# Kernel tuning notes

Hardware: AMD Instinct MI355X
Metric: run time of the kernel (lower is better)

Reference implementation:

```python
import jax, jax.numpy as jnp
import numpy as np

N_NODES = 100000
N_EDGES = 3200000
STATE_DIM = 128
HIDDEN = 256
ACTION_DIM = 64
BN_EPS = 1e-5


def setup_inputs() -> dict:
    key = jax.random.key(0)
    ks = jax.random.split(key, 12)
    feat = jax.random.normal(ks[0], (N_NODES, STATE_DIM), dtype=jnp.float32)
    src = jax.random.randint(ks[1], (N_EDGES,), 0, N_NODES, dtype=jnp.int64) if jax.config.jax_enable_x64 else jax.random.randint(ks[1], (N_EDGES,), 0, N_NODES).astype(jnp.int32)
    dst = jax.random.randint(ks[2], (N_EDGES,), 0, N_NODES).astype(src.dtype)
    def glorot(k, shape):
        lim = np.sqrt(6.0 / (shape[0] + shape[1]))
        return jax.random.uniform(k, shape, jnp.float32, -lim, lim)
    W1 = glorot(ks[3], (STATE_DIM, HIDDEN)); b1 = jnp.zeros((HIDDEN,), jnp.float32)
    W2 = glorot(ks[4], (HIDDEN, HIDDEN));   b2 = jnp.zeros((HIDDEN,), jnp.float32)
    g1 = jnp.ones((HIDDEN,), jnp.float32);  be1 = jnp.zeros((HIDDEN,), jnp.float32)
    g2 = jnp.ones((HIDDEN,), jnp.float32);  be2 = jnp.zeros((HIDDEN,), jnp.float32)
    Wa = glorot(ks[5], (HIDDEN, ACTION_DIM)); ba = jnp.zeros((ACTION_DIM,), jnp.float32)
    Wv = glorot(ks[6], (HIDDEN, 1));          bv = jnp.zeros((1,), jnp.float32)
    return {"feat": feat, "src": src, "dst": dst, "W1": W1, "b1": b1, "g1": g1, "be1": be1,
            "W2": W2, "b2": b2, "g2": g2, "be2": be2, "Wa": Wa, "ba": ba, "Wv": Wv, "bv": bv}


def _graph_conv(x, src, dst, dnorm_out, dnorm_in, W, b):
    # DGL GraphConv, norm='both': scale by out-deg^{-1/2} at src, sum-aggregate at dst,
    # scale by in-deg^{-1/2}, then linear.
    m = x * dnorm_out[:, None]                     # [N, F]
    agg = jax.ops.segment_sum(m[src], dst, num_segments=N_NODES)  # SpMM
    h = agg * dnorm_in[:, None]
    return h @ W + b


def _bn_relu(x, gamma, beta):
    mu = x.mean(axis=0)
    var = x.var(axis=0)  # biased, matches torch BN training normalization
    return jax.nn.relu((x - mu) * jax.lax.rsqrt(var + BN_EPS) * gamma + beta)


def reference(feat, src, dst, W1, b1, g1, be1, W2, b2, g2, be2, Wa, ba, Wv, bv):
    ones = jnp.ones((src.shape[0],), feat.dtype)
    deg_out = jax.ops.segment_sum(ones, src, num_segments=N_NODES)
    deg_in = jax.ops.segment_sum(ones, dst, num_segments=N_NODES)
    dnorm_out = jax.lax.rsqrt(jnp.clip(deg_out, 1.0))
    dnorm_in = jax.lax.rsqrt(jnp.clip(deg_in, 1.0))
    h = _bn_relu(_graph_conv(feat, src, dst, dnorm_out, dnorm_in, W1, b1), g1, be1)
    h = _bn_relu(_graph_conv(h, src, dst, dnorm_out, dnorm_in, W2, b2), g2, be2)
    adv = h @ Wa + ba                              # [N, A]
    val = h @ Wv + bv                              # [N, 1]
    Q = val + (adv - adv.mean(axis=1, keepdims=True))
    return Q
```

## Files before the change

### kernel.cpp

```cpp
#include <hip/hip_runtime.h>
#include <hip/hip_bf16.h>

#define NN 100000
#define NE 3200000
#define HID 256
#define SDIM 128
#define ADIM 64
#define BN_EPS 1e-5f

#define BSH 9
#define NB 196
#define EPB 8192
#define NAB 391

typedef __attribute__((ext_vector_type(8))) short short8;
typedef __attribute__((ext_vector_type(4))) float f32x4;

__device__ __forceinline__ void atomAdd(float* p, float v) { unsafeAtomicAdd(p, v); }
__device__ __forceinline__ float bf2f(ushort u) {
    union { unsigned i; float f; } c; c.i = ((unsigned)u) << 16; return c.f;
}
__device__ __forceinline__ ushort f2bf(float x) {
    __hip_bfloat16 h = __float2bfloat16(x);
    return *reinterpret_cast<ushort*>(&h);
}

__global__ __launch_bounds__(1024)
void k_hist(const int* __restrict__ src, const int* __restrict__ dst,
            unsigned* __restrict__ gh_d, unsigned* __restrict__ gh_s, int E) {
    __shared__ unsigned hd[NB], hs[NB];
    int tid = threadIdx.x;
    if (tid < NB) { hd[tid] = 0; hs[tid] = 0; }
    __syncthreads();
    int base = blockIdx.x * EPB;
    int cnt = min(EPB, E - base);
    for (int i = tid; i < cnt; i += 1024) {
        atomicAdd(&hd[dst[base + i] >> BSH], 1u);
        atomicAdd(&hs[src[base + i] >> BSH], 1u);
    }
    __syncthreads();
    if (tid < NB) {
        if (hd[tid]) atomicAdd(&gh_d[tid * 16], hd[tid]);
        if (hs[tid]) atomicAdd(&gh_s[tid * 16], hs[tid]);
    }
}

__global__ __launch_bounds__(256)
void k_scan_b(const unsigned* __restrict__ gh_d, const unsigned* __restrict__ gh_s,
              unsigned* __restrict__ gcur_d, unsigned* __restrict__ gcur_s,
              unsigned* __restrict__ bbase_d, unsigned* __restrict__ bbase_s,
              int* __restrict__ row_ptr) {
    __shared__ unsigned v[256];
    int t = threadIdx.x;
    unsigned x = (t < NB) ? gh_d[t * 16] : 0;
    v[t] = x; __syncthreads();
    for (int off = 1; off < 256; off <<= 1) {
        unsigned a = (t >= off) ? v[t - off] : 0;
        __syncthreads(); v[t] += a; __syncthreads();
    }
    if (t < NB) { bbase_d[t] = v[t] - x; gcur_d[t * 16] = v[t] - x; }
    if (t == 255) { bbase_d[NB] = v[255]; row_ptr[NN] = (int)v[255]; }
    __syncthreads();
    unsigned y = (t < NB) ? gh_s[t * 16] : 0;
    v[t] = y; __syncthreads();
    for (int off = 1; off < 256; off <<= 1) {
        unsigned a = (t >= off) ? v[t - off] : 0;
        __syncthreads(); v[t] += a; __syncthreads();
    }
    if (t < NB) { bbase_s[t] = v[t] - y; gcur_s[t * 16] = v[t] - y; }
    if (t == 255) bbase_s[NB] = v[255];
}

__global__ __launch_bounds__(1024)
void k_part(const int* __restrict__ src, const int* __restrict__ dst,
            unsigned* __restrict__ gcur_d, unsigned* __restrict__ gcur_s,
            unsigned* __restrict__ outd, ushort* __restrict__ outs, int E) {
    __shared__ unsigned hd[NB], hs[NB], ld_[NB], ls_[NB], cd[NB], cs[NB], bd[NB], bs[NB];
    __shared__ unsigned sv[256];
    __shared__ unsigned stage_d[EPB];
    __shared__ ushort stage_s[EPB];
    __shared__ unsigned char sbd[EPB], sbs[EPB];
    const int tid = threadIdx.x;
    const int base = blockIdx.x * EPB;
    const int cnt = min(EPB, E - base);
    if (tid < NB) { hd[tid] = 0; hs[tid] = 0; }
    __syncthreads();

    int es[8], ed[8];
    #pragma unroll
    for (int i = 0; i < 8; ++i) {
        int g = tid + i * 1024;
        if (g < cnt) { es[i] = src[base + g]; ed[i] = dst[base + g]; }
        else { es[i] = -1; ed[i] = -1; }
    }
    #pragma unroll
    for (int i = 0; i < 8; ++i)
        if (ed[i] >= 0) {
            atomicAdd(&hd[ed[i] >> BSH], 1u);
            atomicAdd(&hs[es[i] >> BSH], 1u);
        }
    __syncthreads();

    {
        unsigned x = (tid < NB) ? hd[tid] : 0;
        if (tid < 256) sv[tid] = x;
        __syncthreads();
        for (int off = 1; off < 256; off <<= 1) {
            unsigned a = 0;
            if (tid < 256 && tid >= off) a = sv[tid - off];
            __syncthreads();
            if (tid < 256) sv[tid] += a;
            __syncthreads();
        }
        if (tid < NB) {
            ld_[tid] = sv[tid] - x; cd[tid] = sv[tid] - x;
            bd[tid] = atomicAdd(&gcur_d[tid * 16], hd[tid]);
        }
        __syncthreads();
        unsigned y = (tid < NB) ? hs[tid] : 0;
        if (tid < 256) sv[tid] = y;
        __syncthreads();
        for (int off = 1; off < 256; off <<= 1) {
            unsigned a = 0;
            if (tid < 256 && tid >= off) a = sv[tid - off];
            __syncthreads();
            if (tid < 256) sv[tid] += a;
            __syncthreads();
        }
        if (tid < NB) {
            ls_[tid] = sv[tid] - y; cs[tid] = sv[tid] - y;
            bs[tid] = atomicAdd(&gcur_s[tid * 16], hs[tid]);
        }
        __syncthreads();
    }

    #pragma unroll
    for (int i = 0; i < 8; ++i)
        if (ed[i] >= 0) {
            int b = ed[i] >> BSH;
            unsigned p = atomicAdd(&cd[b], 1u);
            stage_d[p] = ((unsigned)(ed[i] & ((1 << BSH) - 1)) << 17) | (unsigned)es[i];
            sbd[p] = (unsigned char)b;
            int b2 = es[i] >> BSH;
            unsigned p2 = atomicAdd(&cs[b2], 1u);
            stage_s[p2] = (ushort)(es[i] & ((1 << BSH) - 1));
            sbs[p2] = (unsigned char)b2;
        }
    __syncthreads();

    for (int i = tid; i < cnt; i += 1024) {
        unsigned b = sbd[i];
        outd[bd[b] + (unsigned)i - ld_[b]] = stage_d[i];
        unsigned b2 = sbs[i];
        outs[bs[b2] + (unsigned)i - ls_[b2]] = stage_s[i];
    }
}

__global__ __launch_bounds__(1024)
void k_csr(const unsigned* __restrict__ outd, const unsigned* __restrict__ bbase_d,
           int* __restrict__ row_ptr, int* __restrict__ csr_src, float* __restrict__ dni) {
    __shared__ unsigned h[512], sc[512];
    const int tid = threadIdx.x, b = blockIdx.x;
    const unsigned beg = bbase_d[b], end = bbase_d[b + 1];
    const int cnt = (int)(end - beg);
    if (tid < 512) h[tid] = 0;
    __syncthreads();
    for (int i = tid; i < cnt; i += 1024) atomicAdd(&h[outd[beg + i] >> 17], 1u);
    __syncthreads();
    unsigned my = 0;
    if (tid < 512) { my = h[tid]; sc[tid] = my; }
    __syncthreads();
    for (int off = 1; off < 512; off <<= 1) {
        unsigned a = 0;
        if (tid < 512 && tid >= off) a = sc[tid - off];
        __syncthreads();
        if (tid < 512) sc[tid] += a;
        __syncthreads();
    }
    const int n0 = b << BSH;
    const int nb = min(512, NN - n0);
    unsigned excl = 0;
    if (tid < 512) excl = sc[tid] - my;
    __syncthreads();
    if (tid < 512) h[tid] = excl;
    if (tid < nb) {
        row_ptr[n0 + tid] = (int)(beg + excl);
        dni[n0 + tid] = rsqrtf(fmaxf((float)my, 1.0f));
    }
    __syncthreads();
    for (int i = tid; i < cnt; i += 1024) {
        unsigned p = outd[beg + i];
        unsigned pos = atomicAdd(&h[p >> 17], 1u);
        csr_src[beg + pos] = (int)(p & 0x1FFFFu);
    }
}

__global__ __launch_bounds__(1024)
void k_degout_ps(const ushort* __restrict__ outs, const unsigned* __restrict__ bbase_s,
                 const float* __restrict__ feat, float* __restrict__ dno,
                 ushort* __restrict__ Xb) {
    __shared__ unsigned h[512];
    __shared__ float dnl[512];
    const int tid = threadIdx.x, b = blockIdx.x;
    const unsigned beg = bbase_s[b], end = bbase_s[b + 1];
    const int cnt = (int)(end - beg);
    if (tid < 512) h[tid] = 0;
    __syncthreads();
    for (int i = tid; i < cnt; i += 1024) atomicAdd(&h[outs[beg + i]], 1u);
    __syncthreads();
    const int n0 = b << BSH;
    const int nb = min(512, NN - n0);
    if (tid < nb) {
        float d = rsqrtf(fmaxf((float)h[tid], 1.0f));
        dno[n0 + tid] = d;
        dnl[tid] = d;
    }
    __syncthreads();
    const int total4 = nb * 32;
    for (int slot = tid; slot < total4; slot += 1024) {
        int r = slot >> 5, c4 = slot & 31;
        float s = dnl[r];
        float4 v = reinterpret_cast<const float4*>(feat)[(size_t)(n0 + r) * 32 + c4];
        ushort4 o;
        o.x = f2bf(v.x * s); o.y = f2bf(v.y * s);
        o.z = f2bf(v.z * s); o.w = f2bf(v.w * s);
        reinterpret_cast<ushort4*>(Xb)[(size_t)(n0 + r) * 32 + c4] = o;
    }
}

__global__ __launch_bounds__(256)
void k_wprep(const float* __restrict__ W1, const float* __restrict__ W2,
             const float* __restrict__ Wa, const float* __restrict__ Wv,
             ushort* __restrict__ Wt1, ushort* __restrict__ Wt2, ushort* __restrict__ Wh) {
    int idx = blockIdx.x * 256 + threadIdx.x;
    if (idx < HID * SDIM) {
        int n = idx / SDIM, k = idx - n * SDIM;
        Wt1[idx] = f2bf(W1[(size_t)k * HID + n]);
    } else if (idx < HID * SDIM + HID * HID) {
        int j = idx - HID * SDIM;
        int n = j / HID, k = j - n * HID;
        Wt2[j] = f2bf(W2[(size_t)k * HID + n]);
    } else if (idx < HID * SDIM + HID * HID + 80 * HID) {
        int j = idx - HID * SDIM - HID * HID;
        int n = j / HID, k = j - n * HID;
        float v = 0.f;
        if (n < ADIM) v = Wa[(size_t)k * ADIM + n];
        else if (n == ADIM) v = Wv[k];
        Wh[j] = f2bf(v);
    }
}

template <int F>
__global__ __launch_bounds__(256)
void k_spmm_bf16(const int* __restrict__ row_ptr, const int* __restrict__ csr_src,
                 const ushort* __restrict__ X, const float* __restrict__ dni,
                 ushort* __restrict__ Y, int N) {
    const int node = blockIdx.x * 4 + (threadIdx.x >> 6);
    if (node >= N) return;
    const int lane = threadIdx.x & 63;
    const int beg = row_ptr[node];
    const int end = row_ptr[node + 1];
    float acc[4] = {0.f, 0.f, 0.f, 0.f};

    if (F == 256) {
        const ushort* Xl = X + lane * 4;
        int e = beg;
        for (; e + 1 < end; e += 2) {
            int s0 = csr_src[e];
            int s1 = csr_src[e + 1];
            ushort4 v0 = *reinterpret_cast<const ushort4*>(Xl + (size_t)s0 * 256);
            ushort4 v1 = *reinterpret_cast<const ushort4*>(Xl + (size_t)s1 * 256);
            acc[0] += bf2f(v0.x) + bf2f(v1.x);
            acc[1] += bf2f(v0.y) + bf2f(v1.y);
            acc[2] += bf2f(v0.z) + bf2f(v1.z);
            acc[3] += bf2f(v0.w) + bf2f(v1.w);
        }
        if (e < end) {
            int s0 = csr_src[e];
            ushort4 v0 = *reinterpret_cast<const ushort4*>(Xl + (size_t)s0 * 256);
            acc[0] += bf2f(v0.x); acc[1] += bf2f(v0.y);
            acc[2] += bf2f(v0.z); acc[3] += bf2f(v0.w);
        }
        float wi = dni[node];
        ushort4 o;
        o.x = f2bf(acc[0] * wi); o.y = f2bf(acc[1] * wi);
        o.z = f2bf(acc[2] * wi); o.w = f2bf(acc[3] * wi);
        *reinterpret_cast<ushort4*>(Y + (size_t)node * 256 + lane * 4) = o;
    } else {
        const int half = lane >> 5;
        const int l = lane & 31;
        const ushort* Xl = X + l * 4;
        for (int e = beg + half; e < end; e += 2) {
            int s = csr_src[e];
            ushort4 v = *reinterpret_cast<const ushort4*>(Xl + (size_t)s * 128);
            acc[0] += bf2f(v.x); acc[1] += bf2f(v.y);
            acc[2] += bf2f(v.z); acc[3] += bf2f(v.w);
        }
        acc[0] += __shfl_xor(acc[0], 32);
        acc[1] += __shfl_xor(acc[1], 32);
        acc[2] += __shfl_xor(acc[2], 32);
        acc[3] += __shfl_xor(acc[3], 32);
        if (half == 0) {
            float wi = dni[node];
            ushort4 o;
            o.x = f2bf(acc[0] * wi); o.y = f2bf(acc[1] * wi);
            o.z = f2bf(acc[2] * wi); o.w = f2bf(acc[3] * wi);
            *reinterpret_cast<ushort4*>(Y + (size_t)node * 128 + l * 4) = o;
        }
    }
}

template <int K>
__global__ __launch_bounds__(256, 2)
void k_gemm_mfma(const ushort* __restrict__ A, const ushort* __restrict__ Wt,
                 const float* __restrict__ bias, ushort* __restrict__ outb,
                 float* __restrict__ stats, int M) {
    __shared__ ushort As[128][40];
    __shared__ ushort Bs[256][40];
    __shared__ float sred[4][2][128];
    const int tid = threadIdx.x;
    const int w = tid >> 6;
    const int lane = tid & 63;
    const int wr = (w >> 1) * 64;
    const int wc = (w & 1) * 128;
    const int row0 = blockIdx.x * 128;
    f32x4 acc[4][8] = {};

    const int frow = lane & 15;
    const int fk = (lane >> 4) * 8;

    for (int k0 = 0; k0 < K; k0 += 32) {
        #pragma unroll
        for (int h = 0; h < 2; ++h) {
            int slot = tid + 256 * h;
            int r = slot >> 2;
            int c = (slot & 3) * 8;
            int row = row0 + r;
            int4 v = make_int4(0, 0, 0, 0);
            if (row < M) v = *reinterpret_cast<const int4*>(A + (size_t)row * K + k0 + c);
            *reinterpret_cast<int4*>(&As[r][c]) = v;
        }
        #pragma unroll
        for (int h = 0; h < 4; ++h) {
            int slot = tid + 256 * h;
            int n = slot >> 2;
            int c = (slot & 3) * 8;
            int4 v = *reinterpret_cast<const int4*>(Wt + (size_t)n * K + k0 + c);
            *reinterpret_cast<int4*>(&Bs[n][c]) = v;
        }
        __syncthreads();

        short8 afr[4], bfr[8];
        #pragma unroll
        for (int mi = 0; mi < 4; ++mi)
            afr[mi] = *reinterpret_cast<const short8*>(&As[wr + mi * 16 + frow][fk]);
        #pragma unroll
        for (int ni = 0; ni < 8; ++ni)
            bfr[ni] = *reinterpret_cast<const short8*>(&Bs[wc + ni * 16 + frow][fk]);
        #pragma unroll
        for (int mi = 0; mi < 4; ++mi)
            #pragma unroll
            for (int ni = 0; ni < 8; ++ni)
                acc[mi][ni] = __builtin_amdgcn_mfma_f32_16x16x32_bf16(afr[mi], bfr[ni], acc[mi][ni], 0, 0, 0);
        __syncthreads();
    }

    const int ncol = lane & 15;
    const int rbase = (lane >> 4) * 4;
    #pragma unroll
    for (int ni = 0; ni < 8; ++ni) {
        int col = wc + ni * 16 + ncol;
        float b = bias[col];
        float s1 = 0.f, s2 = 0.f;
        #pragma unroll
        for (int mi = 0; mi < 4; ++mi) {
            #pragma unroll
            for (int q = 0; q < 4; ++q) {
                int row = row0 + wr + mi * 16 + rbase + q;
                if (row < M) {
                    float val = acc[mi][ni][q] + b;
                    outb[(size_t)row * HID + col] = f2bf(val);
                    s1 += val;
                    s2 += val * val;
                }
            }
        }
        s1 += __shfl_xor(s1, 16); s1 += __shfl_xor(s1, 32);
        s2 += __shfl_xor(s2, 16); s2 += __shfl_xor(s2, 32);
        if ((lane >> 4) == 0) {
            sred[w][0][ni * 16 + ncol] = s1;
            sred[w][1][ni * 16 + ncol] = s2;
        }
    }
    __syncthreads();
    {
        int c = tid;
        int half = c >> 7, cl = c & 127;
        float v0 = sred[half][0][cl] + sred[half + 2][0][cl];
        float v1 = sred[half][1][cl] + sred[half + 2][1][cl];
        atomAdd(&stats[c], v0);
        atomAdd(&stats[HID + c], v1);
    }
}

__global__ __launch_bounds__(256)
void k_bn_relu_ps(const ushort* __restrict__ Gb, const float* __restrict__ stats,
                  const float* __restrict__ gamma, const float* __restrict__ beta,
                  const float* __restrict__ dno, ushort* __restrict__ Y, int total8) {
    int idx = blockIdx.x * 256 + threadIdx.x;
    if (idx >= total8) return;
    int row = idx >> 5;
    int c0 = (idx & 31) * 8;
    short8 v = *reinterpret_cast<const short8*>(Gb + (size_t)idx * 8);
    float s = dno[row];
    float inv_n = 1.0f / (float)NN;
    short8 o;
    #pragma unroll
    for (int j = 0; j < 8; ++j) {
        int c = c0 + j;
        float mean = stats[c] * inv_n;
        float var = stats[HID + c] * inv_n - mean * mean;
        float sc = gamma[c] * rsqrtf(var + BN_EPS);
        float sh = beta[c] - mean * sc;
        float x = bf2f((ushort)v[j]);
        float y = fmaf(x, sc, sh);
        y = y > 0.f ? y : 0.f;
        o[j] = (short)f2bf(y * s);
    }
    *reinterpret_cast<short8*>(Y + (size_t)idx * 8) = o;
}

__global__ __launch_bounds__(256)
void k_bn_qhead(const ushort* __restrict__ Gb, const float* __restrict__ stats,
                const float* __restrict__ gamma, const float* __restrict__ beta,
                const ushort* __restrict__ Wh, const float* __restrict__ ba,
                const float* __restrict__ bv, float* __restrict__ out, int M) {
    __shared__ ushort As[128][40];
    __shared__ ushort Bs[80][264];
    __shared__ float sc_s[HID], sh_s[HID];
    const int tid = threadIdx.x;
    const int w = tid >> 6;
    const int lane = tid & 63;
    const int row0 = blockIdx.x * 128;
    const int frow = lane & 15;
    const int fk8 = (lane >> 4) * 8;

    {
        float inv_n = 1.0f / (float)NN;
        float mean = stats[tid] * inv_n;
        float var = stats[HID + tid] * inv_n - mean * mean;
        float sc = gamma[tid] * rsqrtf(var + BN_EPS);
        sc_s[tid] = sc;
        sh_s[tid] = beta[tid] - mean * sc;
    }
    #pragma unroll
    for (int h = 0; h < 10; ++h) {
        int slot = tid + 256 * h;
        int n = slot >> 5;
        int c = (slot & 31) * 8;
        int4 v = *reinterpret_cast<const int4*>(Wh + (size_t)n * HID + c);
        *reinterpret_cast<int4*>(&Bs[n][c]) = v;
    }
    __syncthreads();

    f32x4 acc[2][5] = {};
    for (int k0 = 0; k0 < HID; k0 += 32) {
        #pragma unroll
        for (int h = 0; h < 2; ++h) {
            int slot = tid + 256 * h;
            int r = slot >> 2;
            int c = (slot & 3) * 8;
            int row = row0 + r;
            short8 o = {};
            if (row < M) {
                short8 v = *reinterpret_cast<const short8*>(Gb + (size_t)row * HID + k0 + c);
                #pragma unroll
                for (int j = 0; j < 8; ++j) {
                    int k = k0 + c + j;
                    float y = fmaf(bf2f((ushort)v[j]), sc_s[k], sh_s[k]);
                    o[j] = (short)f2bf(y > 0.f ? y : 0.f);
                }
            }
            *reinterpret_cast<short8*>(&As[r][c]) = o;
        }
        __syncthreads();
        short8 afr[2], bfr[5];
        #pragma unroll
        for (int mi = 0; mi < 2; ++mi)
            afr[mi] = *reinterpret_cast<const short8*>(&As[w * 32 + mi * 16 + frow][fk8]);
        #pragma unroll
        for (int ni = 0; ni < 5; ++ni)
            bfr[ni] = *reinterpret_cast<const short8*>(&Bs[ni * 16 + frow][k0 + fk8]);
        #pragma unroll
        for (int mi = 0; mi < 2; ++mi)
            #pragma unroll
            for (int ni = 0; ni < 5; ++ni)
                acc[mi][ni] = __builtin_amdgcn_mfma_f32_16x16x32_bf16(afr[mi], bfr[ni], acc[mi][ni], 0, 0, 0);
        __syncthreads();
    }

    const int ncol = lane & 15;
    const int gb = lane & 48;
    const float bv0 = bv[0];
    float ba_l[4];
    #pragma unroll
    for (int ni = 0; ni < 4; ++ni) ba_l[ni] = ba[ni * 16 + ncol];
    #pragma unroll
    for (int mi = 0; mi < 2; ++mi) {
        #pragma unroll
        for (int q = 0; q < 4; ++q) {
            int row = row0 + w * 32 + mi * 16 + (lane >> 4) * 4 + q;
            float adv[4];
            float s = 0.f;
            #pragma unroll
            for (int ni = 0; ni < 4; ++ni) {
                adv[ni] = acc[mi][ni][q] + ba_l[ni];
                s += adv[ni];
            }
            s += __shfl_xor(s, 1); s += __shfl_xor(s, 2);
            s += __shfl_xor(s, 4); s += __shfl_xor(s, 8);
            float mean = s * (1.0f / ADIM);
            float val = acc[mi][4][q] + bv0;
            val = __shfl(val, gb);
            if (row < M) {
                #pragma unroll
                for (int ni = 0; ni < 4; ++ni)
                    out[(size_t)row * ADIM + ni * 16 + ncol] = val + adv[ni] - mean;
            }
        }
    }
}

extern "C" void kernel_launch(void* const* d_in, const int* in_sizes, int n_in,
                              void* d_out, int out_size, void* d_ws, size_t ws_size,
                              hipStream_t stream) {
    const float* feat = (const float*)d_in[0];
    const int* src = (const int*)d_in[1];
    const int* dst = (const int*)d_in[2];
    const float* W1 = (const float*)d_in[3];
    const float* b1 = (const float*)d_in[4];
    const float* g1 = (const float*)d_in[5];
    const float* be1 = (const float*)d_in[6];
    const float* W2 = (const float*)d_in[7];
    const float* b2 = (const float*)d_in[8];
    const float* g2 = (const float*)d_in[9];
    const float* be2 = (const float*)d_in[10];
    const float* Wa = (const float*)d_in[11];
    const float* ba = (const float*)d_in[12];
    const float* Wv = (const float*)d_in[13];
    const float* bv = (const float*)d_in[14];
    float* out = (float*)d_out;

    char* w = (char*)d_ws;
    unsigned* gh_d   = (unsigned*)w;  w += (size_t)NB * 16 * 4;
    unsigned* gh_s   = (unsigned*)w;  w += (size_t)NB * 16 * 4;
    float* stats     = (float*)w;     w += 1024 * 4;
    unsigned* gcur_d = (unsigned*)w;  w += (size_t)NB * 16 * 4;
    unsigned* gcur_s = (unsigned*)w;  w += (size_t)NB * 16 * 4;
    unsigned* bbase_d= (unsigned*)w;  w += (NB + 4) * 4;
    unsigned* bbase_s= (unsigned*)w;  w += (NB + 4) * 4;
    float* dn_out    = (float*)w;     w += (size_t)NN * 4;
    float* dn_in     = (float*)w;     w += (size_t)NN * 4;
    int* row_ptr     = (int*)w;       w += (size_t)(NN + 4) * 4;
    unsigned* outd   = (unsigned*)w;  w += (size_t)NE * 4;
    ushort* outs     = (ushort*)w;    w += (size_t)NE * 2;
    int* csr_src     = (int*)w;       w += (size_t)NE * 4;
    ushort* Wt1      = (ushort*)w;    w += (size_t)HID * SDIM * 2;
    ushort* Wt2      = (ushort*)w;    w += (size_t)HID * HID * 2;
    ushort* Whb      = (ushort*)w;    w += (size_t)80 * HID * 2;
    ushort* Xb       = (ushort*)w;    w += (size_t)NN * HID * 2;
    ushort* Ab       = (ushort*)w;    w += (size_t)NN * HID * 2;
    ushort* Gb       = (ushort*)w;    w += (size_t)NN * HID * 2;

    hipMemsetAsync(gh_d, 0, (size_t)2 * NB * 16 * 4 + 1024 * 4, stream);

    {
        int total = HID * SDIM + HID * HID + 80 * HID;
        k_wprep<<<(total + 255) / 256, 256, 0, stream>>>(W1, W2, Wa, Wv, Wt1, Wt2, Whb);
    }

    k_hist<<<NAB, 1024, 0, stream>>>(src, dst, gh_d, gh_s, NE);
    k_scan_b<<<1, 256, 0, stream>>>(gh_d, gh_s, gcur_d, gcur_s, bbase_d, bbase_s, row_ptr);
    k_part<<<NAB, 1024, 0, stream>>>(src, dst, gcur_d, gcur_s, outd, outs, NE);
    k_csr<<<NB, 1024, 0, stream>>>(outd, bbase_d, row_ptr, csr_src, dn_in);
    k_degout_ps<<<NB, 1024, 0, stream>>>(outs, bbase_s, feat, dn_out, Xb);

    const int gblocks = (NN + 127) / 128;

    {
        k_spmm_bf16<SDIM><<<(NN + 3) / 4, 256, 0, stream>>>(row_ptr, csr_src, Xb, dn_in, Ab, NN);
        k_gemm_mfma<SDIM><<<gblocks, 256, 0, stream>>>(Ab, Wt1, b1, Gb, stats, NN);
        int t8 = NN * (HID / 8);
        k_bn_relu_ps<<<(t8 + 255) / 256, 256, 0, stream>>>(Gb, stats, g1, be1, dn_out, Xb, t8);
    }

    {
        k_spmm_bf16<HID><<<(NN + 3) / 4, 256, 0, stream>>>(row_ptr, csr_src, Xb, dn_in, Ab, NN);
        k_gemm_mfma<HID><<<gblocks, 256, 0, stream>>>(Ab, Wt2, b2, Gb, stats + 512, NN);
        k_bn_qhead<<<gblocks, 256, 0, stream>>>(Gb, stats + 512, g2, be2, Whb, ba, bv, out, NN);
    }
}
```

Before: 749.7 us.

## Fuse BN+ReLU+degree scaling into layer-2 SpMM gather and use wave-shuffle scans

Measured after the change: 716.7 us. 1.05x faster.

```diff
diff --git a/kernel.cpp b/kernel.cpp
--- a/kernel.cpp
+++ b/kernel.cpp
@@ -10,8 +10,8 @@
 
 #define BSH 9
 #define NB 196
-#define EPB 8192
-#define NAB 391
+#define EPB 16384
+#define NAB 196
 
 typedef __attribute__((ext_vector_type(8))) short short8;
 typedef __attribute__((ext_vector_type(4))) float f32x4;
@@ -23,6 +23,16 @@
 __device__ __forceinline__ ushort f2bf(float x) {
     __hip_bfloat16 h = __float2bfloat16(x);
     return *reinterpret_cast<ushort*>(&h);
+}
+
+__device__ __forceinline__ unsigned wave_excl_scan(unsigned t, int lane) {
+    unsigned p = t;
+    #pragma unroll
+    for (int d = 1; d < 64; d <<= 1) {
+        unsigned q = __shfl_up(p, d);
+        if (lane >= d) p += q;
+    }
+    return p - t;
 }
 
 __global__ __launch_bounds__(1024)
@@ -76,7 +86,6 @@
             unsigned* __restrict__ gcur_d, unsigned* __restrict__ gcur_s,
             unsigned* __restrict__ outd, ushort* __restrict__ outs, int E) {
     __shared__ unsigned hd[NB], hs[NB], ld_[NB], ls_[NB], cd[NB], cs[NB], bd[NB], bs[NB];
-    __shared__ unsigned sv[256];
     __shared__ unsigned stage_d[EPB];
     __shared__ ushort stage_s[EPB];
     __shared__ unsigned char sbd[EPB], sbs[EPB];
@@ -86,15 +95,15 @@
     if (tid < NB) { hd[tid] = 0; hs[tid] = 0; }
     __syncthreads();
 
-    int es[8], ed[8];
-    #pragma unroll
-    for (int i = 0; i < 8; ++i) {
+    int es[16], ed[16];
+    #pragma unroll
+    for (int i = 0; i < 16; ++i) {
         int g = tid + i * 1024;
         if (g < cnt) { es[i] = src[base + g]; ed[i] = dst[base + g]; }
         else { es[i] = -1; ed[i] = -1; }
     }
     #pragma unroll
-    for (int i = 0; i < 8; ++i)
+    for (int i = 0; i < 16; ++i)
         if (ed[i] >= 0) {
             atomicAdd(&hd[ed[i] >> BSH], 1u);
             atomicAdd(&hs[es[i] >> BSH], 1u);
@@ -102,40 +111,45 @@
     __syncthreads();
 
     {
-        unsigned x = (tid < NB) ? hd[tid] : 0;
-        if (tid < 256) sv[tid] = x;
-        __syncthreads();
-        for (int off = 1; off < 256; off <<= 1) {
-            unsigned a = 0;
-            if (tid < 256 && tid >= off) a = sv[tid - off];
-            __syncthreads();
-            if (tid < 256) sv[tid] += a;
-            __syncthreads();
-        }
-        if (tid < NB) {
-            ld_[tid] = sv[tid] - x; cd[tid] = sv[tid] - x;
-            bd[tid] = atomicAdd(&gcur_d[tid * 16], hd[tid]);
-        }
-        __syncthreads();
-        unsigned y = (tid < NB) ? hs[tid] : 0;
-        if (tid < 256) sv[tid] = y;
-        __syncthreads();
-        for (int off = 1; off < 256; off <<= 1) {
-            unsigned a = 0;
-            if (tid < 256 && tid >= off) a = sv[tid - off];
-            __syncthreads();
-            if (tid < 256) sv[tid] += a;
-            __syncthreads();
-        }
-        if (tid < NB) {
-            ls_[tid] = sv[tid] - y; cs[tid] = sv[tid] - y;
-            bs[tid] = atomicAdd(&gcur_s[tid * 16], hs[tid]);
-        }
-        __syncthreads();
-    }
-
-    #pragma unroll
-    for (int i = 0; i < 8; ++i)
+        const int wv = tid >> 6, lane = tid & 63;
+        if (wv == 0) {
+            unsigned v[4]; unsigned t = 0;
+            #pragma unroll
+            for (int j = 0; j < 4; ++j) {
+                int i = lane * 4 + j;
+                v[j] = (i < NB) ? hd[i] : 0; t += v[j];
+            }
+            unsigned excl = wave_excl_scan(t, lane);
+            #pragma unroll
+            for (int j = 0; j < 4; ++j) {
+                int i = lane * 4 + j;
+                if (i < NB) { ld_[i] = excl; cd[i] = excl; }
+                excl += v[j];
+            }
+        } else if (wv == 1) {
+            unsigned v[4]; unsigned t = 0;
+            #pragma unroll
+            for (int j = 0; j < 4; ++j) {
+                int i = lane * 4 + j;
+                v[j] = (i < NB) ? hs[i] : 0; t += v[j];
+            }
+            unsigned excl = wave_excl_scan(t, lane);
+            #pragma unroll
+            for (int j = 0; j < 4; ++j) {
+                int i = lane * 4 + j;
+                if (i < NB) { ls_[i] = excl; cs[i] = excl; }
+                excl += v[j];
+            }
+        } else if (wv == 2) {
+            for (int i = lane; i < NB; i += 64) bd[i] = atomicAdd(&gcur_d[i * 16], hd[i]);
+        } else if (wv == 3) {
+            for (int i = lane; i < NB; i += 64) bs[i] = atomicAdd(&gcur_s[i * 16], hs[i]);
+        }
+    }
+    __syncthreads();
+
+    #pragma unroll
+    for (int i = 0; i < 16; ++i)
         if (ed[i] >= 0) {
             int b = ed[i] >> BSH;
             unsigned p = atomicAdd(&cd[b], 1u);
@@ -167,30 +181,26 @@
     __syncthreads();
     for (int i = tid; i < cnt; i += 1024) atomicAdd(&h[outd[beg + i] >> 17], 1u);
     __syncthreads();
-    unsigned my = 0;
-    if (tid < 512) { my = h[tid]; sc[tid] = my; }
-    __syncthreads();
-    for (int off = 1; off < 512; off <<= 1) {
-        unsigned a = 0;
-        if (tid < 512 && tid >= off) a = sc[tid - off];
-        __syncthreads();
-        if (tid < 512) sc[tid] += a;
-        __syncthreads();
-    }
+    if (tid < 64) {
+        const int lane = tid;
+        unsigned v[8]; unsigned t = 0;
+        #pragma unroll
+        for (int j = 0; j < 8; ++j) { v[j] = h[lane * 8 + j]; t += v[j]; }
+        unsigned excl = wave_excl_scan(t, lane);
+        #pragma unroll
+        for (int j = 0; j < 8; ++j) { sc[lane * 8 + j] = excl; excl += v[j]; }
+    }
+    __syncthreads();
     const int n0 = b << BSH;
     const int nb = min(512, NN - n0);
-    unsigned excl = 0;
-    if (tid < 512) excl = sc[tid] - my;
-    __syncthreads();
-    if (tid < 512) h[tid] = excl;
     if (tid < nb) {
-        row_ptr[n0 + tid] = (int)(beg + excl);
-        dni[n0 + tid] = rsqrtf(fmaxf((float)my, 1.0f));
+        row_ptr[n0 + tid] = (int)(beg + sc[tid]);
+        dni[n0 + tid] = rsqrtf(fmaxf((float)h[tid], 1.0f));
     }
     __syncthreads();
     for (int i = tid; i < cnt; i += 1024) {
         unsigned p = outd[beg + i];
-        unsigned pos = atomicAdd(&h[p >> 17], 1u);
+        unsigned pos = atomicAdd(&sc[p >> 17], 1u);
         csr_src[beg + pos] = (int)(p & 0x1FFFFu);
     }
 }
@@ -250,64 +260,103 @@
     }
 }
 
-template <int F>
 __global__ __launch_bounds__(256)
-void k_spmm_bf16(const int* __restrict__ row_ptr, const int* __restrict__ csr_src,
-                 const ushort* __restrict__ X, const float* __restrict__ dni,
-                 ushort* __restrict__ Y, int N) {
+void k_spmm_l1(const int* __restrict__ row_ptr, const int* __restrict__ csr_src,
+               const ushort* __restrict__ X, const float* __restrict__ dni,
+               ushort* __restrict__ Y, int N) {
     const int node = blockIdx.x * 4 + (threadIdx.x >> 6);
     if (node >= N) return;
     const int lane = threadIdx.x & 63;
     const int beg = row_ptr[node];
     const int end = row_ptr[node + 1];
     float acc[4] = {0.f, 0.f, 0.f, 0.f};
-
-    if (F == 256) {
-        const ushort* Xl = X + lane * 4;
-        int e = beg;
-        for (; e + 1 < end; e += 2) {
-            int s0 = csr_src[e];
-            int s1 = csr_src[e + 1];
-            ushort4 v0 = *reinterpret_cast<const ushort4*>(Xl + (size_t)s0 * 256);
-            ushort4 v1 = *reinterpret_cast<const ushort4*>(Xl + (size_t)s1 * 256);
-            acc[0] += bf2f(v0.x) + bf2f(v1.x);
-            acc[1] += bf2f(v0.y) + bf2f(v1.y);
-            acc[2] += bf2f(v0.z) + bf2f(v1.z);
-            acc[3] += bf2f(v0.w) + bf2f(v1.w);
-        }
-        if (e < end) {
-            int s0 = csr_src[e];
-            ushort4 v0 = *reinterpret_cast<const ushort4*>(Xl + (size_t)s0 * 256);
-            acc[0] += bf2f(v0.x); acc[1] += bf2f(v0.y);
-            acc[2] += bf2f(v0.z); acc[3] += bf2f(v0.w);
-        }
+    const int half = lane >> 5;
+    const int l = lane & 31;
+    const ushort* Xl = X + l * 4;
+    for (int e = beg + half; e < end; e += 2) {
+        int s = csr_src[e];
+        ushort4 v = *reinterpret_cast<const ushort4*>(Xl + (size_t)s * 128);
+        acc[0] += bf2f(v.x); acc[1] += bf2f(v.y);
+        acc[2] += bf2f(v.z); acc[3] += bf2f(v.w);
+    }
+    acc[0] += __shfl_xor(acc[0], 32);
+    acc[1] += __shfl_xor(acc[1], 32);
+    acc[2] += __shfl_xor(acc[2], 32);
+    acc[3] += __shfl_xor(acc[3], 32);
+    if (half == 0) {
         float wi = dni[node];
         ushort4 o;
         o.x = f2bf(acc[0] * wi); o.y = f2bf(acc[1] * wi);
         o.z = f2bf(acc[2] * wi); o.w = f2bf(acc[3] * wi);
-        *reinterpret_cast<ushort4*>(Y + (size_t)node * 256 + lane * 4) = o;
-    } else {
-        const int half = lane >> 5;
-        const int l = lane & 31;
-        const ushort* Xl = X + l * 4;
-        for (int e = beg + half; e < end; e += 2) {
-            int s = csr_src[e];
-            ushort4 v = *reinterpret_cast<const ushort4*>(Xl + (size_t)s * 128);
-            acc[0] += bf2f(v.x); acc[1] += bf2f(v.y);
-            acc[2] += bf2f(v.z); acc[3] += bf2f(v.w);
-        }
-        acc[0] += __shfl_xor(acc[0], 32);
-        acc[1] += __shfl_xor(acc[1], 32);
-        acc[2] += __shfl_xor(acc[2], 32);
-        acc[3] += __shfl_xor(acc[3], 32);
-        if (half == 0) {
-            float wi = dni[node];
-            ushort4 o;
-            o.x = f2bf(acc[0] * wi); o.y = f2bf(acc[1] * wi);
-            o.z = f2bf(acc[2] * wi); o.w = f2bf(acc[3] * wi);
-            *reinterpret_cast<ushort4*>(Y + (size_t)node * 128 + l * 4) = o;
-        }
-    }
+        *reinterpret_cast<ushort4*>(Y + (size_t)node * 128 + l * 4) = o;
+    }
+}
+
+__global__ __launch_bounds__(256)
+void k_spmm_bn(const int* __restrict__ row_ptr, const int* __restrict__ csr_src,
+               const ushort* __restrict__ Gb, const float* __restrict__ stats,
+               const float* __restrict__ gamma, const float* __restrict__ beta,
+               const float* __restrict__ dno, const float* __restrict__ dni,
+               ushort* __restrict__ Y, int N) {
+    __shared__ float sc_s[HID], sh_s[HID];
+    {
+        int c = threadIdx.x;
+        float inv_n = 1.0f / (float)NN;
+        float mean = stats[c] * inv_n;
+        float var = stats[HID + c] * inv_n - mean * mean;
+        float sc = gamma[c] * rsqrtf(var + BN_EPS);
+        sc_s[c] = sc;
+        sh_s[c] = beta[c] - mean * sc;
+    }
+    __syncthreads();
+    const int node = blockIdx.x * 4 + (threadIdx.x >> 6);
+    if (node >= N) return;
+    const int lane = threadIdx.x & 63;
+    const int c0 = lane * 4;
+    float sc[4], sh[4];
+    #pragma unroll
+    for (int j = 0; j < 4; ++j) { sc[j] = sc_s[c0 + j]; sh[j] = sh_s[c0 + j]; }
+    const int beg = row_ptr[node];
+    const int end = row_ptr[node + 1];
+    float acc[4] = {0.f, 0.f, 0.f, 0.f};
+    const ushort* Gl = Gb + c0;
+    int e = beg;
+    for (; e + 1 < end; e += 2) {
+        int s0 = csr_src[e];
+        int s1 = csr_src[e + 1];
+        float w0 = dno[s0];
+        float w1 = dno[s1];
+        ushort4 v0 = *reinterpret_cast<const ushort4*>(Gl + (size_t)s0 * 256);
+        ushort4 v1 = *reinterpret_cast<const ushort4*>(Gl + (size_t)s1 * 256);
+        const ushort* p0 = &v0.x;
+        const ushort* p1 = &v1.x;
+        #pragma unroll
+        for (int j = 0; j < 4; ++j) {
+            float y0 = fmaf(bf2f(p0[j]), sc[j], sh[j]);
+            y0 = y0 > 0.f ? y0 : 0.f;
+            acc[j] = fmaf(y0, w0, acc[j]);
+            float y1 = fmaf(bf2f(p1[j]), sc[j], sh[j]);
+            y1 = y1 > 0.f ? y1 : 0.f;
+            acc[j] = fmaf(y1, w1, acc[j]);
+        }
+    }
+    if (e < end) {
+        int s0 = csr_src[e];
+        float w0 = dno[s0];
+        ushort4 v0 = *reinterpret_cast<const ushort4*>(Gl + (size_t)s0 * 256);
+        const ushort* p0 = &v0.x;
+        #pragma unroll
+        for (int j = 0; j < 4; ++j) {
+            float y0 = fmaf(bf2f(p0[j]), sc[j], sh[j]);
+            y0 = y0 > 0.f ? y0 : 0.f;
+            acc[j] = fmaf(y0, w0, acc[j]);
+        }
+    }
+    float wi = dni[node];
+    ushort4 o;
+    o.x = f2bf(acc[0] * wi); o.y = f2bf(acc[1] * wi);
+    o.z = f2bf(acc[2] * wi); o.w = f2bf(acc[3] * wi);
+    *reinterpret_cast<ushort4*>(Y + (size_t)node * 256 + c0) = o;
 }
 
 template <int K>
@@ -401,33 +450,6 @@
         atomAdd(&stats[c], v0);
         atomAdd(&stats[HID + c], v1);
     }
-}
-
-__global__ __launch_bounds__(256)
-void k_bn_relu_ps(const ushort* __restrict__ Gb, const float* __restrict__ stats,
-                  const float* __restrict__ gamma, const float* __restrict__ beta,
-                  const float* __restrict__ dno, ushort* __restrict__ Y, int total8) {
-    int idx = blockIdx.x * 256 + threadIdx.x;
-    if (idx >= total8) return;
-    int row = idx >> 5;
-    int c0 = (idx & 31) * 8;
-    short8 v = *reinterpret_cast<const short8*>(Gb + (size_t)idx * 8);
-    float s = dno[row];
-    float inv_n = 1.0f / (float)NN;
-    short8 o;
-    #pragma unroll
-    for (int j = 0; j < 8; ++j) {
-        int c = c0 + j;
-        float mean = stats[c] * inv_n;
-        float var = stats[HID + c] * inv_n - mean * mean;
-        float sc = gamma[c] * rsqrtf(var + BN_EPS);
-        float sh = beta[c] - mean * sc;
-        float x = bf2f((ushort)v[j]);
-        float y = fmaf(x, sc, sh);
-        y = y > 0.f ? y : 0.f;
-        o[j] = (short)f2bf(y * s);
-    }
-    *reinterpret_cast<short8*>(Y + (size_t)idx * 8) = o;
 }
 
 __global__ __launch_bounds__(256)
@@ -568,7 +590,7 @@
     ushort* Wt1      = (ushort*)w;    w += (size_t)HID * SDIM * 2;
     ushort* Wt2      = (ushort*)w;    w += (size_t)HID * HID * 2;
     ushort* Whb      = (ushort*)w;    w += (size_t)80 * HID * 2;
-    ushort* Xb       = (ushort*)w;    w += (size_t)NN * HID * 2;
+    ushort* Xb       = (ushort*)w;    w += (size_t)NN * SDIM * 2;
     ushort* Ab       = (ushort*)w;    w += (size_t)NN * HID * 2;
     ushort* Gb       = (ushort*)w;    w += (size_t)NN * HID * 2;
 
@@ -587,16 +609,11 @@
 
     const int gblocks = (NN + 127) / 128;
 
-    {
-        k_spmm_bf16<SDIM><<<(NN + 3) / 4, 256, 0, stream>>>(row_ptr, csr_src, Xb, dn_in, Ab, NN);
-        k_gemm_mfma<SDIM><<<gblocks, 256, 0, stream>>>(Ab, Wt1, b1, Gb, stats, NN);
-        int t8 = NN * (HID / 8);
-        k_bn_relu_ps<<<(t8 + 255) / 256, 256, 0, stream>>>(Gb, stats, g1, be1, dn_out, Xb, t8);
-    }
-
-    {
-        k_spmm_bf16<HID><<<(NN + 3) / 4, 256, 0, stream>>>(row_ptr, csr_src, Xb, dn_in, Ab, NN);
-        k_gemm_mfma<HID><<<gblocks, 256, 0, stream>>>(Ab, Wt2, b2, Gb, stats + 512, NN);
-        k_bn_qhead<<<gblocks, 256, 0, stream>>>(Gb, stats + 512, g2, be2, Whb, ba, bv, out, NN);
-    }
-}
+    k_spmm_l1<<<(NN + 3) / 4, 256, 0, stream>>>(row_ptr, csr_src, Xb, dn_in, Ab, NN);
+    k_gemm_mfma<SDIM><<<gblocks, 256, 0, stream>>>(Ab, Wt1, b1, Gb, stats, NN);
+
+    k_spmm_bn<<<(NN + 3) / 4, 256, 0, stream>>>(row_ptr, csr_src, Gb, stats, g1, be1,
+                                                dn_out, dn_in, Ab, NN);
+    k_gemm_mfma<HID><<<gblocks, 256, 0, stream>>>(Ab, Wt2, b2, Gb, stats + 512, NN);
+    k_bn_qhead<<<gblocks, 256, 0, stream>>>(Gb, stats + 512, g2, be2, Whb, ba, bv, out, NN);
+}
```
